# Optimization experiments

Measured on AMD Instinct MI355X. Metric: run time of the kernel, lower is better.

Reference implementation:

```python
import jax, jax.numpy as jnp
import numpy as np

N = 100000      # nodes
E = 1600000     # edges (before self-loops)
F_DIM = 256     # feat_dim
H = 64          # hidden_dim
EPS = 1e-5      # BatchNorm eps
NEG_SLOPE = 0.2 # PyG GATConv leaky_relu slope


def _glorot(key, shape):
    fan_in, fan_out = shape[0], shape[-1]
    s = jnp.sqrt(2.0 / (fan_in + fan_out)).astype(jnp.float32)
    return jax.random.normal(key, shape, dtype=jnp.float32) * s


def setup_inputs() -> dict:
    key = jax.random.key(0)
    ks = jax.random.split(key, 16)
    inp = {
        "feat": jax.random.normal(ks[0], (N, F_DIM), dtype=jnp.float32),
        "edge_index": jax.random.randint(ks[1], (2, E), 0, N, dtype=jnp.int64)
        if jax.config.jax_enable_x64 else jax.random.randint(ks[1], (2, E), 0, N).astype(jnp.int32),
    }
    dims = [(F_DIM, H), (H, H), (H, H), (H, F_DIM)]  # gc1-enc, gc2-enc, gc1-dec, gc2-dec
    for i, (din, dout) in enumerate(dims, start=1):
        k = jax.random.split(ks[1 + i], 4)
        inp[f"W{i}"] = _glorot(k[0], (din, dout))
        inp[f"as{i}"] = _glorot(k[1], (dout,))
        inp[f"ad{i}"] = _glorot(k[2], (dout,))
        inp[f"bi{i}"] = jnp.zeros((dout,), dtype=jnp.float32)
    # BatchNorm affine params (eval mode: running_mean=0, running_var=1)
    for i in range(1, 4):
        inp[f"g{i}"] = jnp.ones((H,), dtype=jnp.float32)
        inp[f"be{i}"] = jnp.zeros((H,), dtype=jnp.float32)
    return inp


def _gat(x, src, dst, W, a_src, a_dst, b, n):
    # PyG single-head GATConv: h = xW; e_ij = LeakyReLU(a_s.h_i + a_d.h_j);
    # alpha = softmax over edges sharing a destination; out_j = sum alpha_ij h_i + b
    h = x @ W                                   # [N, dout]
    e = jax.nn.leaky_relu((h @ a_src)[src] + (h @ a_dst)[dst], NEG_SLOPE)  # [Etot]
    m = jax.ops.segment_max(e, dst, num_segments=n)
    m = jnp.where(jnp.isfinite(m), m, 0.0)
    p = jnp.exp(e - m[dst])
    denom = jax.ops.segment_sum(p, dst, num_segments=n)
    alpha = p / (denom[dst] + 1e-16)
    out = jax.ops.segment_sum(alpha[:, None] * h[src], dst, num_segments=n)
    return out + b


def _bn_eval(x, gamma, beta):
    # eval-mode BatchNorm1d with running_mean=0, running_var=1
    return x * (gamma / jnp.sqrt(1.0 + EPS)) + beta


def reference(feat, edge_index,
              W1, as1, ad1, bi1, W2, as2, ad2, bi2,
              W3, as3, ad3, bi3, W4, as4, ad4, bi4,
              g1, be1, g2, be2, g3, be3):
    n = feat.shape[0]
    loops = jnp.arange(n, dtype=edge_index.dtype)
    src = jnp.concatenate([edge_index[0], loops])  # add_self_loops=True
    dst = jnp.concatenate([edge_index[1], loops])
    # GraphEncoder
    x = jax.nn.relu(_gat(feat, src, dst, W1, as1, ad1, bi1, n))
    x = _bn_eval(x, g1, be1)  # dropout inactive (eval)
    x = jax.nn.relu(_gat(x, src, dst, W2, as2, ad2, bi2, n))
    x = _bn_eval(x, g2, be2)
    # AttributeDecoder
    x = jax.nn.relu(_gat(x, src, dst, W3, as3, ad3, bi3, n))
    x = _bn_eval(x, g3, be3)
    x = jax.nn.relu(_gat(x, src, dst, W4, as4, ad4, bi4, n))
    return x
```

## Files before the change

kernel.cpp:

```cpp
#include <hip/hip_runtime.h>
#include <cmath>

#define SLOPE 0.2f
#define EPSV 1e-5f

__global__ __launch_bounds__(256) void deg_init_kernel(int* __restrict__ deg, int n) {
    int i = blockIdx.x * 256 + threadIdx.x;
    if (i <= n) deg[i] = (i < n) ? 1 : 0;
}

__global__ __launch_bounds__(256) void hist_kernel(const int* __restrict__ dst, int E,
                                                   int* __restrict__ deg) {
    int stride = gridDim.x * 256;
    for (int e = blockIdx.x * 256 + threadIdx.x; e < E; e += stride)
        atomicAdd(&deg[dst[e]], 1);
}

__global__ __launch_bounds__(256) void scan_block_kernel(const int* __restrict__ deg,
                                                         int* __restrict__ row,
                                                         int* __restrict__ partials, int n1) {
    __shared__ int s[256];
    int t = threadIdx.x;
    int i = blockIdx.x * 256 + t;
    int v = (i < n1) ? deg[i] : 0;
    s[t] = v;
    __syncthreads();
    for (int off = 1; off < 256; off <<= 1) {
        int x = (t >= off) ? s[t - off] : 0;
        __syncthreads();
        s[t] += x;
        __syncthreads();
    }
    if (i < n1) row[i] = s[t] - v;
    if (t == 255) partials[blockIdx.x] = s[255];
}

__global__ __launch_bounds__(1024) void scan_top_kernel(int* __restrict__ partials, int nb) {
    __shared__ int s[1024];
    int t = threadIdx.x;
    int v = (t < nb) ? partials[t] : 0;
    s[t] = v;
    __syncthreads();
    for (int off = 1; off < 1024; off <<= 1) {
        int x = (t >= off) ? s[t - off] : 0;
        __syncthreads();
        s[t] += x;
        __syncthreads();
    }
    if (t < nb) partials[t] = s[t] - v;
}

__global__ __launch_bounds__(256) void scan_add_kernel(int* __restrict__ row,
                                                       const int* __restrict__ partials, int n1) {
    int i = blockIdx.x * 256 + threadIdx.x;
    if (i < n1) row[i] += partials[blockIdx.x];
}

__global__ __launch_bounds__(256) void fill_self_kernel(const int* __restrict__ row,
                                                        int* __restrict__ cursor,
                                                        int* __restrict__ csr, int n) {
    int i = blockIdx.x * 256 + threadIdx.x;
    if (i < n) {
        int p = row[i];
        csr[p] = i;
        cursor[i] = p + 1;
    }
}

__global__ __launch_bounds__(256) void fill_edge_kernel(const int* __restrict__ src,
                                                        const int* __restrict__ dst, int E,
                                                        int* __restrict__ cursor,
                                                        int* __restrict__ csr) {
    int stride = gridDim.x * 256;
    for (int e = blockIdx.x * 256 + threadIdx.x; e < E; e += stride) {
        int p = atomicAdd(&cursor[dst[e]], 1);
        csr[p] = src[e];
    }
}

template <int DIN>
__device__ __forceinline__ float dot1(const float* __restrict__ Ws,
                                      const float* __restrict__ X, int node, int lane) {
    const float4* xr = reinterpret_cast<const float4*>(X + (size_t)node * DIN);
    float acc = 0.f;
#pragma unroll 8
    for (int k4 = 0; k4 < DIN / 4; ++k4) {
        float4 x4 = xr[k4];
        acc = fmaf(x4.x, Ws[(4 * k4 + 0) * 64 + lane], acc);
        acc = fmaf(x4.y, Ws[(4 * k4 + 1) * 64 + lane], acc);
        acc = fmaf(x4.z, Ws[(4 * k4 + 2) * 64 + lane], acc);
        acc = fmaf(x4.w, Ws[(4 * k4 + 3) * 64 + lane], acc);
    }
    return acc;
}

template <int DIN>
__global__ __launch_bounds__(256) void gemm_scores_kernel(
    const float* __restrict__ X, const float* __restrict__ W,
    const float* __restrict__ a_s, const float* __restrict__ a_d,
    float* __restrict__ H, float* __restrict__ s_src, float* __restrict__ s_dst, int n) {
    __shared__ float Ws[DIN * 64];
    const float4* W4 = reinterpret_cast<const float4*>(W);
    float4* Ws4 = reinterpret_cast<float4*>(Ws);
    for (int i = threadIdx.x; i < DIN * 16; i += 256) Ws4[i] = W4[i];
    __syncthreads();

    const int lane = threadIdx.x & 63;
    const int wv = threadIdx.x >> 6;
    const float as_l = a_s[lane];
    const float ad_l = a_d[lane];
    const int stride = gridDim.x * 16;

    for (int base = (blockIdx.x * 4 + wv) * 4; base < n; base += stride) {
        if (base + 4 <= n) {
            const float4* x0 = reinterpret_cast<const float4*>(X + (size_t)(base + 0) * DIN);
            const float4* x1 = reinterpret_cast<const float4*>(X + (size_t)(base + 1) * DIN);
            const float4* x2 = reinterpret_cast<const float4*>(X + (size_t)(base + 2) * DIN);
            const float4* x3 = reinterpret_cast<const float4*>(X + (size_t)(base + 3) * DIN);
            float acc0 = 0.f, acc1 = 0.f, acc2 = 0.f, acc3 = 0.f;
#pragma unroll 8
            for (int k4 = 0; k4 < DIN / 4; ++k4) {
                float4 a = x0[k4], b = x1[k4], c = x2[k4], d = x3[k4];
                float w0 = Ws[(4 * k4 + 0) * 64 + lane];
                float w1 = Ws[(4 * k4 + 1) * 64 + lane];
                float w2 = Ws[(4 * k4 + 2) * 64 + lane];
                float w3 = Ws[(4 * k4 + 3) * 64 + lane];
                acc0 = fmaf(a.x, w0, fmaf(a.y, w1, fmaf(a.z, w2, fmaf(a.w, w3, acc0))));
                acc1 = fmaf(b.x, w0, fmaf(b.y, w1, fmaf(b.z, w2, fmaf(b.w, w3, acc1))));
                acc2 = fmaf(c.x, w0, fmaf(c.y, w1, fmaf(c.z, w2, fmaf(c.w, w3, acc2))));
                acc3 = fmaf(d.x, w0, fmaf(d.y, w1, fmaf(d.z, w2, fmaf(d.w, w3, acc3))));
            }
            H[(size_t)(base + 0) * 64 + lane] = acc0;
            H[(size_t)(base + 1) * 64 + lane] = acc1;
            H[(size_t)(base + 2) * 64 + lane] = acc2;
            H[(size_t)(base + 3) * 64 + lane] = acc3;
            float p0s = acc0 * as_l, p0d = acc0 * ad_l;
            float p1s = acc1 * as_l, p1d = acc1 * ad_l;
            float p2s = acc2 * as_l, p2d = acc2 * ad_l;
            float p3s = acc3 * as_l, p3d = acc3 * ad_l;
#pragma unroll
            for (int off = 32; off; off >>= 1) {
                p0s += __shfl_xor(p0s, off); p0d += __shfl_xor(p0d, off);
                p1s += __shfl_xor(p1s, off); p1d += __shfl_xor(p1d, off);
                p2s += __shfl_xor(p2s, off); p2d += __shfl_xor(p2d, off);
                p3s += __shfl_xor(p3s, off); p3d += __shfl_xor(p3d, off);
            }
            if (lane == 0) {
                s_src[base + 0] = p0s; s_dst[base + 0] = p0d;
                s_src[base + 1] = p1s; s_dst[base + 1] = p1d;
                s_src[base + 2] = p2s; s_dst[base + 2] = p2d;
                s_src[base + 3] = p3s; s_dst[base + 3] = p3d;
            }
        } else {
            for (int node = base; node < n; ++node) {
                float acc = dot1<DIN>(Ws, X, node, lane);
                H[(size_t)node * 64 + lane] = acc;
                float ps = acc * as_l, pd = acc * ad_l;
#pragma unroll
                for (int off = 32; off; off >>= 1) {
                    ps += __shfl_xor(ps, off);
                    pd += __shfl_xor(pd, off);
                }
                if (lane == 0) { s_src[node] = ps; s_dst[node] = pd; }
            }
        }
    }
}

__global__ __launch_bounds__(256) void scores_x_kernel(
    const float* __restrict__ X, const float* __restrict__ Was,
    const float* __restrict__ Wad, float* __restrict__ s_src,
    float* __restrict__ s_dst, int n) {
    const int lane = threadIdx.x & 63;
    const int node = (blockIdx.x * 256 + threadIdx.x) >> 6;
    if (node >= n) return;
    float x = X[(size_t)node * 64 + lane];
    float ps = x * Was[lane];
    float pd = x * Wad[lane];
#pragma unroll
    for (int off = 32; off; off >>= 1) {
        ps += __shfl_xor(ps, off);
        pd += __shfl_xor(pd, off);
    }
    if (lane == 0) {
        s_src[node] = ps;
        s_dst[node] = pd;
    }
}

__global__ __launch_bounds__(128) void wa_kernel(const float* __restrict__ W ,
                                                 const float* __restrict__ a_s,
                                                 const float* __restrict__ a_d,
                                                 float* __restrict__ Was,
                                                 float* __restrict__ Wad) {
    int t = threadIdx.x;
    int k = t & 63;
    const float* a = (t < 64) ? a_s : a_d;
    float* o = (t < 64) ? Was : Wad;
    const float4* wr = reinterpret_cast<const float4*>(W + (size_t)k * 256);
    const float4* a4 = reinterpret_cast<const float4*>(a);
    float acc = 0.f;
#pragma unroll
    for (int j = 0; j < 64; ++j) {
        float4 w = wr[j];
        float4 av = a4[j];
        acc = fmaf(w.x, av.x, acc);
        acc = fmaf(w.y, av.y, acc);
        acc = fmaf(w.z, av.z, acc);
        acc = fmaf(w.w, av.w, acc);
    }
    o[k] = acc;
}

template <int MODE>
__global__ __launch_bounds__(256) void gather_kernel(
    const int* __restrict__ row, const int* __restrict__ csr,
    const float* __restrict__ s_src, const float* __restrict__ s_dst,
    const float* __restrict__ H, const float* __restrict__ bi,
    const float* __restrict__ g, const float* __restrict__ be,
    float* __restrict__ Out, int n) {
    const int lane = threadIdx.x & 63;
    const int node = (blockIdx.x * 256 + threadIdx.x) >> 6;
    if (node >= n) return;
    const int beg = row[node];
    const int end = row[node + 1];
    const int deg = end - beg;
    const float sdd = s_dst[node];

    const int e0 = beg + lane;
    int c0 = 0;
    float v0 = -1e30f;
    bool has0 = (e0 < end);
    if (has0) {
        c0 = csr[e0];
        float t = s_src[c0] + sdd;
        v0 = t >= 0.f ? t : SLOPE * t;
    }
    float m = v0;
    float dl = has0 ? 1.f : 0.f;
    for (int e = e0 + 64; e < end; e += 64) {
        int s = csr[e];
        float t = s_src[s] + sdd;
        t = t >= 0.f ? t : SLOPE * t;
        float nm = fmaxf(m, t);
        dl = dl * __expf(m - nm) + __expf(t - nm);
        m = nm;
    }
    float M = m;
#pragma unroll
    for (int off = 32; off; off >>= 1) M = fmaxf(M, __shfl_xor(M, off));
    dl *= __expf(m - M);
#pragma unroll
    for (int off = 32; off; off >>= 1) dl += __shfl_xor(dl, off);
    const float invden = 1.f / (dl + 1e-16f);
    const float p0 = has0 ? __expf(v0 - M) : 0.f;

    float acc = 0.f;
    const int nf = deg < 64 ? deg : 64;
    int k = 0;
    for (; k + 8 <= nf; k += 8) {
        int s0 = __shfl(c0, k + 0), s1 = __shfl(c0, k + 1);
        int s2 = __shfl(c0, k + 2), s3 = __shfl(c0, k + 3);
        int s4 = __shfl(c0, k + 4), s5 = __shfl(c0, k + 5);
        int s6 = __shfl(c0, k + 6), s7 = __shfl(c0, k + 7);
        float a0 = __shfl(p0, k + 0), a1 = __shfl(p0, k + 1);
        float a2 = __shfl(p0, k + 2), a3 = __shfl(p0, k + 3);
        float a4 = __shfl(p0, k + 4), a5 = __shfl(p0, k + 5);
        float a6 = __shfl(p0, k + 6), a7 = __shfl(p0, k + 7);
        float h0 = H[(size_t)s0 * 64 + lane], h1 = H[(size_t)s1 * 64 + lane];
        float h2 = H[(size_t)s2 * 64 + lane], h3 = H[(size_t)s3 * 64 + lane];
        float h4 = H[(size_t)s4 * 64 + lane], h5 = H[(size_t)s5 * 64 + lane];
        float h6 = H[(size_t)s6 * 64 + lane], h7 = H[(size_t)s7 * 64 + lane];
        acc = fmaf(a0, h0, acc); acc = fmaf(a1, h1, acc);
        acc = fmaf(a2, h2, acc); acc = fmaf(a3, h3, acc);
        acc = fmaf(a4, h4, acc); acc = fmaf(a5, h5, acc);
        acc = fmaf(a6, h6, acc); acc = fmaf(a7, h7, acc);
    }
    for (; k < nf; ++k) {
        int s = __shfl(c0, k);
        float a = __shfl(p0, k);
        acc = fmaf(a, H[(size_t)s * 64 + lane], acc);
    }
    for (int e = beg + 64; e < end; ++e) {
        int s = csr[e];
        float t = s_src[s] + sdd;
        t = t >= 0.f ? t : SLOPE * t;
        acc = fmaf(__expf(t - M), H[(size_t)s * 64 + lane], acc);
    }
    acc *= invden;

    float o;
    if (MODE == 0) {
        o = fmaxf(acc + bi[lane], 0.f) * (g[lane] * rsqrtf(1.f + EPSV)) + be[lane];
    } else {
        o = acc;
    }
    Out[(size_t)node * 64 + lane] = o;
}

__global__ __launch_bounds__(256) void gemm_out_kernel(const float* __restrict__ X,
                                                       const float* __restrict__ W,
                                                       const float* __restrict__ bi,
                                                       float* __restrict__ Out, int n) {
    const int j = threadIdx.x;
    float wcol[64];
#pragma unroll
    for (int k = 0; k < 64; ++k) wcol[k] = W[k * 256 + j];
    const float bj = bi[j];
    for (int node = blockIdx.x; node < n; node += gridDim.x) {
        const float4* xr = reinterpret_cast<const float4*>(X + (size_t)node * 64);
        float acc = 0.f;
#pragma unroll
        for (int k4 = 0; k4 < 16; ++k4) {
            float4 x4 = xr[k4];
            acc = fmaf(x4.x, wcol[4 * k4 + 0],
                  fmaf(x4.y, wcol[4 * k4 + 1],
                  fmaf(x4.z, wcol[4 * k4 + 2],
                  fmaf(x4.w, wcol[4 * k4 + 3], acc))));
        }
        Out[(size_t)node * 256 + j] = fmaxf(acc + bj, 0.f);
    }
}

extern "C" void kernel_launch(void* const* d_in, const int* in_sizes, int n_in,
                              void* d_out, int out_size, void* d_ws,
                              size_t ws_size, hipStream_t stream) {
    const float* feat = (const float*)d_in[0];
    const int* eidx = (const int*)d_in[1];
    const float* W[4] = {(const float*)d_in[2], (const float*)d_in[6],
                         (const float*)d_in[10], (const float*)d_in[14]};
    const float* As[4] = {(const float*)d_in[3], (const float*)d_in[7],
                          (const float*)d_in[11], (const float*)d_in[15]};
    const float* Ad[4] = {(const float*)d_in[4], (const float*)d_in[8],
                          (const float*)d_in[12], (const float*)d_in[16]};
    const float* Bi[4] = {(const float*)d_in[5], (const float*)d_in[9],
                          (const float*)d_in[13], (const float*)d_in[17]};
    const float* G[3] = {(const float*)d_in[18], (const float*)d_in[20],
                         (const float*)d_in[22]};
    const float* Be[3] = {(const float*)d_in[19], (const float*)d_in[21],
                          (const float*)d_in[23]};

    const int N = in_sizes[0] / 256;
    const int E = in_sizes[1] / 2;
    const int* srcA = eidx;
    const int* dstA = eidx + E;

    float* h = (float*)d_ws;
    float* xA = h + (size_t)N * 64;
    float* xB = xA + (size_t)N * 64;
    float* s_src = xB + (size_t)N * 64;
    float* s_dst = s_src + N;
    float* Was = s_dst + N;
    float* Wad = Was + 64;
    int* deg = (int*)(Wad + 64);
    int* row = deg + (N + 1);
    int* cursor = row + (N + 1);
    int* partials = cursor + N;
    int* csr = partials + 1024;

    const int n1 = N + 1;
    const int NB1 = (n1 + 255) / 256;
    const int node_grid = (N + 3) / 4;
    (void)ws_size; (void)n_in; (void)out_size;

    deg_init_kernel<<<NB1, 256, 0, stream>>>(deg, N);
    hist_kernel<<<2048, 256, 0, stream>>>(dstA, E, deg);
    scan_block_kernel<<<NB1, 256, 0, stream>>>(deg, row, partials, n1);
    scan_top_kernel<<<1, 1024, 0, stream>>>(partials, NB1);
    scan_add_kernel<<<NB1, 256, 0, stream>>>(row, partials, n1);
    fill_self_kernel<<<NB1, 256, 0, stream>>>(row, cursor, csr, N);
    fill_edge_kernel<<<2048, 256, 0, stream>>>(srcA, dstA, E, cursor, csr);

    gemm_scores_kernel<256><<<512, 256, 0, stream>>>(
        feat, W[0], As[0], Ad[0], h, s_src, s_dst, N);
    gather_kernel<0><<<node_grid, 256, 0, stream>>>(
        row, csr, s_src, s_dst, h, Bi[0], G[0], Be[0], xA, N);

    gemm_scores_kernel<64><<<1024, 256, 0, stream>>>(
        xA, W[1], As[1], Ad[1], h, s_src, s_dst, N);
    gather_kernel<0><<<node_grid, 256, 0, stream>>>(
        row, csr, s_src, s_dst, h, Bi[1], G[1], Be[1], xB, N);

    gemm_scores_kernel<64><<<1024, 256, 0, stream>>>(
        xB, W[2], As[2], Ad[2], h, s_src, s_dst, N);
    gather_kernel<0><<<node_grid, 256, 0, stream>>>(
        row, csr, s_src, s_dst, h, Bi[2], G[2], Be[2], xA, N);

    wa_kernel<<<1, 128, 0, stream>>>(W[3], As[3], Ad[3], Was, Wad);
    scores_x_kernel<<<node_grid, 256, 0, stream>>>(xA, Was, Wad, s_src, s_dst, N);
    gather_kernel<1><<<node_grid, 256, 0, stream>>>(
        row, csr, s_src, s_dst, xA, nullptr, nullptr, nullptr, h, N);
    gemm_out_kernel<<<2048, 256, 0, stream>>>(h, W[3], Bi[3], (float*)d_out, N);
}
```

Baseline: 1.108 ms.

## Hold weight columns in registers and split K across waves in layer-1 GEMM

The GEMM+score kernels now keep each lane's 64-entry weight column in registers instead of reading it from LDS. For the 256-wide first layer, each of the four waves handles a 64-wide K slice, and the partial sums are reduced through shared memory, with two barriers per group of 4 nodes. The aim is to remove LDS read traffic and let the weights fit in registers. The cost is higher register pressure, which may lower occupancy, plus extra syncs in the layer-1 kernel, whose grid is raised to 1024 blocks.

After: 1.126 ms. Within noise of the previous version (+1.6%).

```diff
diff --git a/kernel.cpp b/kernel.cpp
--- a/kernel.cpp
+++ b/kernel.cpp
@@ -78,66 +78,98 @@
     }
 }
 
-template <int DIN>
-__device__ __forceinline__ float dot1(const float* __restrict__ Ws,
-                                      const float* __restrict__ X, int node, int lane) {
-    const float4* xr = reinterpret_cast<const float4*>(X + (size_t)node * DIN);
-    float acc = 0.f;
-#pragma unroll 8
-    for (int k4 = 0; k4 < DIN / 4; ++k4) {
-        float4 x4 = xr[k4];
-        acc = fmaf(x4.x, Ws[(4 * k4 + 0) * 64 + lane], acc);
-        acc = fmaf(x4.y, Ws[(4 * k4 + 1) * 64 + lane], acc);
-        acc = fmaf(x4.z, Ws[(4 * k4 + 2) * 64 + lane], acc);
-        acc = fmaf(x4.w, Ws[(4 * k4 + 3) * 64 + lane], acc);
-    }
-    return acc;
-}
-
-template <int DIN>
-__global__ __launch_bounds__(256) void gemm_scores_kernel(
+__global__ __launch_bounds__(256) void gemm_scores256_kernel(
     const float* __restrict__ X, const float* __restrict__ W,
     const float* __restrict__ a_s, const float* __restrict__ a_d,
     float* __restrict__ H, float* __restrict__ s_src, float* __restrict__ s_dst, int n) {
-    __shared__ float Ws[DIN * 64];
-    const float4* W4 = reinterpret_cast<const float4*>(W);
-    float4* Ws4 = reinterpret_cast<float4*>(Ws);
-    for (int i = threadIdx.x; i < DIN * 16; i += 256) Ws4[i] = W4[i];
-    __syncthreads();
-
+    __shared__ float part[4 * 4 * 64];
     const int lane = threadIdx.x & 63;
     const int wv = threadIdx.x >> 6;
+    float wcol[64];
+#pragma unroll
+    for (int k = 0; k < 64; ++k) wcol[k] = W[(wv * 64 + k) * 64 + lane];
     const float as_l = a_s[lane];
     const float ad_l = a_d[lane];
-    const int stride = gridDim.x * 16;
-
-    for (int base = (blockIdx.x * 4 + wv) * 4; base < n; base += stride) {
+
+    for (int base = blockIdx.x * 4; base < n; base += gridDim.x * 4) {
+#pragma unroll
+        for (int g = 0; g < 4; ++g) {
+            const int node = base + g;
+            float acc = 0.f;
+            if (node < n) {
+                const float4* xr =
+                    reinterpret_cast<const float4*>(X + (size_t)node * 256 + wv * 64);
+#pragma unroll
+                for (int k4 = 0; k4 < 16; ++k4) {
+                    float4 x4 = xr[k4];
+                    acc = fmaf(x4.x, wcol[4 * k4 + 0],
+                          fmaf(x4.y, wcol[4 * k4 + 1],
+                          fmaf(x4.z, wcol[4 * k4 + 2],
+                          fmaf(x4.w, wcol[4 * k4 + 3], acc))));
+                }
+            }
+            part[(g * 4 + wv) * 64 + lane] = acc;
+        }
+        __syncthreads();
+        const int node = base + wv;
+        if (node < n) {
+            float h = part[(wv * 4 + 0) * 64 + lane] + part[(wv * 4 + 1) * 64 + lane] +
+                      part[(wv * 4 + 2) * 64 + lane] + part[(wv * 4 + 3) * 64 + lane];
+            H[(size_t)node * 64 + lane] = h;
+            float ps = h * as_l, pd = h * ad_l;
+#pragma unroll
+            for (int off = 32; off; off >>= 1) {
+                ps += __shfl_xor(ps, off);
+                pd += __shfl_xor(pd, off);
+            }
+            if (lane == 0) {
+                s_src[node] = ps;
+                s_dst[node] = pd;
+            }
+        }
+        __syncthreads();
+    }
+}
+
+__global__ __launch_bounds__(256) void gemm_scores64_kernel(
+    const float* __restrict__ X, const float* __restrict__ W,
+    const float* __restrict__ a_s, const float* __restrict__ a_d,
+    float* __restrict__ H, float* __restrict__ s_src, float* __restrict__ s_dst, int n) {
+    const int lane = threadIdx.x & 63;
+    const int wv = threadIdx.x >> 6;
+    float wcol[64];
+#pragma unroll
+    for (int k = 0; k < 64; ++k) wcol[k] = W[k * 64 + lane];
+    const float as_l = a_s[lane];
+    const float ad_l = a_d[lane];
+    const int wid = blockIdx.x * 4 + wv;
+    const int nw = gridDim.x * 4;
+
+    for (int base = wid * 4; base < n; base += nw * 4) {
         if (base + 4 <= n) {
-            const float4* x0 = reinterpret_cast<const float4*>(X + (size_t)(base + 0) * DIN);
-            const float4* x1 = reinterpret_cast<const float4*>(X + (size_t)(base + 1) * DIN);
-            const float4* x2 = reinterpret_cast<const float4*>(X + (size_t)(base + 2) * DIN);
-            const float4* x3 = reinterpret_cast<const float4*>(X + (size_t)(base + 3) * DIN);
-            float acc0 = 0.f, acc1 = 0.f, acc2 = 0.f, acc3 = 0.f;
-#pragma unroll 8
-            for (int k4 = 0; k4 < DIN / 4; ++k4) {
-                float4 a = x0[k4], b = x1[k4], c = x2[k4], d = x3[k4];
-                float w0 = Ws[(4 * k4 + 0) * 64 + lane];
-                float w1 = Ws[(4 * k4 + 1) * 64 + lane];
-                float w2 = Ws[(4 * k4 + 2) * 64 + lane];
-                float w3 = Ws[(4 * k4 + 3) * 64 + lane];
-                acc0 = fmaf(a.x, w0, fmaf(a.y, w1, fmaf(a.z, w2, fmaf(a.w, w3, acc0))));
-                acc1 = fmaf(b.x, w0, fmaf(b.y, w1, fmaf(b.z, w2, fmaf(b.w, w3, acc1))));
-                acc2 = fmaf(c.x, w0, fmaf(c.y, w1, fmaf(c.z, w2, fmaf(c.w, w3, acc2))));
-                acc3 = fmaf(d.x, w0, fmaf(d.y, w1, fmaf(d.z, w2, fmaf(d.w, w3, acc3))));
-            }
-            H[(size_t)(base + 0) * 64 + lane] = acc0;
-            H[(size_t)(base + 1) * 64 + lane] = acc1;
-            H[(size_t)(base + 2) * 64 + lane] = acc2;
-            H[(size_t)(base + 3) * 64 + lane] = acc3;
-            float p0s = acc0 * as_l, p0d = acc0 * ad_l;
-            float p1s = acc1 * as_l, p1d = acc1 * ad_l;
-            float p2s = acc2 * as_l, p2d = acc2 * ad_l;
-            float p3s = acc3 * as_l, p3d = acc3 * ad_l;
+            const float4* x0 = reinterpret_cast<const float4*>(X + (size_t)(base + 0) * 64);
+            const float4* x1 = reinterpret_cast<const float4*>(X + (size_t)(base + 1) * 64);
+            const float4* x2 = reinterpret_cast<const float4*>(X + (size_t)(base + 2) * 64);
+            const float4* x3 = reinterpret_cast<const float4*>(X + (size_t)(base + 3) * 64);
+            float a0 = 0.f, a1 = 0.f, a2 = 0.f, a3 = 0.f;
+#pragma unroll
+            for (int k4 = 0; k4 < 16; ++k4) {
+                float4 xa = x0[k4], xb = x1[k4], xc = x2[k4], xd = x3[k4];
+                float w0 = wcol[4 * k4 + 0], w1 = wcol[4 * k4 + 1];
+                float w2 = wcol[4 * k4 + 2], w3 = wcol[4 * k4 + 3];
+                a0 = fmaf(xa.x, w0, fmaf(xa.y, w1, fmaf(xa.z, w2, fmaf(xa.w, w3, a0))));
+                a1 = fmaf(xb.x, w0, fmaf(xb.y, w1, fmaf(xb.z, w2, fmaf(xb.w, w3, a1))));
+                a2 = fmaf(xc.x, w0, fmaf(xc.y, w1, fmaf(xc.z, w2, fmaf(xc.w, w3, a2))));
+                a3 = fmaf(xd.x, w0, fmaf(xd.y, w1, fmaf(xd.z, w2, fmaf(xd.w, w3, a3))));
+            }
+            H[(size_t)(base + 0) * 64 + lane] = a0;
+            H[(size_t)(base + 1) * 64 + lane] = a1;
+            H[(size_t)(base + 2) * 64 + lane] = a2;
+            H[(size_t)(base + 3) * 64 + lane] = a3;
+            float p0s = a0 * as_l, p0d = a0 * ad_l;
+            float p1s = a1 * as_l, p1d = a1 * ad_l;
+            float p2s = a2 * as_l, p2d = a2 * ad_l;
+            float p3s = a3 * as_l, p3d = a3 * ad_l;
 #pragma unroll
             for (int off = 32; off; off >>= 1) {
                 p0s += __shfl_xor(p0s, off); p0d += __shfl_xor(p0d, off);
@@ -153,7 +185,16 @@
             }
         } else {
             for (int node = base; node < n; ++node) {
-                float acc = dot1<DIN>(Ws, X, node, lane);
+                const float4* xr = reinterpret_cast<const float4*>(X + (size_t)node * 64);
+                float acc = 0.f;
+#pragma unroll
+                for (int k4 = 0; k4 < 16; ++k4) {
+                    float4 x4 = xr[k4];
+                    acc = fmaf(x4.x, wcol[4 * k4 + 0],
+                          fmaf(x4.y, wcol[4 * k4 + 1],
+                          fmaf(x4.z, wcol[4 * k4 + 2],
+                          fmaf(x4.w, wcol[4 * k4 + 3], acc))));
+                }
                 H[(size_t)node * 64 + lane] = acc;
                 float ps = acc * as_l, pd = acc * ad_l;
 #pragma unroll
@@ -371,17 +412,17 @@
     fill_self_kernel<<<NB1, 256, 0, stream>>>(row, cursor, csr, N);
     fill_edge_kernel<<<2048, 256, 0, stream>>>(srcA, dstA, E, cursor, csr);
 
-    gemm_scores_kernel<256><<<512, 256, 0, stream>>>(
+    gemm_scores256_kernel<<<1024, 256, 0, stream>>>(
         feat, W[0], As[0], Ad[0], h, s_src, s_dst, N);
     gather_kernel<0><<<node_grid, 256, 0, stream>>>(
         row, csr, s_src, s_dst, h, Bi[0], G[0], Be[0], xA, N);
 
-    gemm_scores_kernel<64><<<1024, 256, 0, stream>>>(
+    gemm_scores64_kernel<<<1024, 256, 0, stream>>>(
         xA, W[1], As[1], Ad[1], h, s_src, s_dst, N);
     gather_kernel<0><<<node_grid, 256, 0, stream>>>(
         row, csr, s_src, s_dst, h, Bi[1], G[1], Be[1], xB, N);
 
-    gemm_scores_kernel<64><<<1024, 256, 0, stream>>>(
+    gemm_scores64_kernel<<<1024, 256, 0, stream>>>(
         xB, W[2], As[2], Ad[2], h, s_src, s_dst, N);
     gather_kernel<0><<<node_grid, 256, 0, stream>>>(
         row, csr, s_src, s_dst, h, Bi[2], G[2], Be[2], xA, N);
```

## Hold weight columns in registers and tile 16 nodes per wave in GEMMs

Applied to the files above, without the earlier changes.

The dense projection kernels change from staging W in LDS across 256-thread blocks to single-wave blocks. Each block keeps a 64-row slice of a weight column in registers and computes 16 nodes at once, with K tiled for the 256-wide input. The output GEMM is restructured the same way, looping over four 64-column quarters per 16-node group. The aim is to drop LDS reads and block syncs and reuse register weights across nodes, at the cost of heavy register pressure, reloading weights per block, and many tiny blocks.

Result: slower. 1.205 ms (+8.8%).

```diff
diff --git a/kernel.cpp b/kernel.cpp
--- a/kernel.cpp
+++ b/kernel.cpp
@@ -78,91 +78,59 @@
     }
 }
 
-template <int DIN>
-__device__ __forceinline__ float dot1(const float* __restrict__ Ws,
-                                      const float* __restrict__ X, int node, int lane) {
-    const float4* xr = reinterpret_cast<const float4*>(X + (size_t)node * DIN);
-    float acc = 0.f;
-#pragma unroll 8
-    for (int k4 = 0; k4 < DIN / 4; ++k4) {
-        float4 x4 = xr[k4];
-        acc = fmaf(x4.x, Ws[(4 * k4 + 0) * 64 + lane], acc);
-        acc = fmaf(x4.y, Ws[(4 * k4 + 1) * 64 + lane], acc);
-        acc = fmaf(x4.z, Ws[(4 * k4 + 2) * 64 + lane], acc);
-        acc = fmaf(x4.w, Ws[(4 * k4 + 3) * 64 + lane], acc);
-    }
-    return acc;
-}
-
-template <int DIN>
-__global__ __launch_bounds__(256) void gemm_scores_kernel(
+template <int KTILES>
+__global__ __launch_bounds__(64, 4) void gemm_scores_kernel(
     const float* __restrict__ X, const float* __restrict__ W,
     const float* __restrict__ a_s, const float* __restrict__ a_d,
-    float* __restrict__ H, float* __restrict__ s_src, float* __restrict__ s_dst, int n) {
-    __shared__ float Ws[DIN * 64];
-    const float4* W4 = reinterpret_cast<const float4*>(W);
-    float4* Ws4 = reinterpret_cast<float4*>(Ws);
-    for (int i = threadIdx.x; i < DIN * 16; i += 256) Ws4[i] = W4[i];
-    __syncthreads();
-
-    const int lane = threadIdx.x & 63;
-    const int wv = threadIdx.x >> 6;
-    const float as_l = a_s[lane];
-    const float ad_l = a_d[lane];
-    const int stride = gridDim.x * 16;
-
-    for (int base = (blockIdx.x * 4 + wv) * 4; base < n; base += stride) {
-        if (base + 4 <= n) {
-            const float4* x0 = reinterpret_cast<const float4*>(X + (size_t)(base + 0) * DIN);
-            const float4* x1 = reinterpret_cast<const float4*>(X + (size_t)(base + 1) * DIN);
-            const float4* x2 = reinterpret_cast<const float4*>(X + (size_t)(base + 2) * DIN);
-            const float4* x3 = reinterpret_cast<const float4*>(X + (size_t)(base + 3) * DIN);
-            float acc0 = 0.f, acc1 = 0.f, acc2 = 0.f, acc3 = 0.f;
-#pragma unroll 8
-            for (int k4 = 0; k4 < DIN / 4; ++k4) {
-                float4 a = x0[k4], b = x1[k4], c = x2[k4], d = x3[k4];
-                float w0 = Ws[(4 * k4 + 0) * 64 + lane];
-                float w1 = Ws[(4 * k4 + 1) * 64 + lane];
-                float w2 = Ws[(4 * k4 + 2) * 64 + lane];
-                float w3 = Ws[(4 * k4 + 3) * 64 + lane];
-                acc0 = fmaf(a.x, w0, fmaf(a.y, w1, fmaf(a.z, w2, fmaf(a.w, w3, acc0))));
-                acc1 = fmaf(b.x, w0, fmaf(b.y, w1, fmaf(b.z, w2, fmaf(b.w, w3, acc1))));
-                acc2 = fmaf(c.x, w0, fmaf(c.y, w1, fmaf(c.z, w2, fmaf(c.w, w3, acc2))));
-                acc3 = fmaf(d.x, w0, fmaf(d.y, w1, fmaf(d.z, w2, fmaf(d.w, w3, acc3))));
+    float* __restrict__ H, float* __restrict__ s_src, float* __restrict__ s_dst,
+    int n) {
+    const int lane = threadIdx.x;
+    const int base = blockIdx.x * 16;
+    if (base >= n) return;
+
+    float acc[16];
+#pragma unroll
+    for (int g = 0; g < 16; ++g) acc[g] = 0.f;
+
+#pragma unroll 1
+    for (int t = 0; t < KTILES; ++t) {
+        float wcol[64];
+#pragma unroll
+        for (int k = 0; k < 64; ++k) wcol[k] = W[(t * 64 + k) * 64 + lane];
+#pragma unroll
+        for (int g = 0; g < 16; ++g) {
+            const int node = base + g;
+            if (node < n) {
+                const float4* xr = reinterpret_cast<const float4*>(
+                    X + (size_t)node * (KTILES * 64) + t * 64);
+#pragma unroll
+                for (int k4 = 0; k4 < 16; ++k4) {
+                    float4 x4 = xr[k4];
+                    acc[g] = fmaf(x4.x, wcol[4 * k4 + 0],
+                             fmaf(x4.y, wcol[4 * k4 + 1],
+                             fmaf(x4.z, wcol[4 * k4 + 2],
+                             fmaf(x4.w, wcol[4 * k4 + 3], acc[g]))));
+                }
             }
-            H[(size_t)(base + 0) * 64 + lane] = acc0;
-            H[(size_t)(base + 1) * 64 + lane] = acc1;
-            H[(size_t)(base + 2) * 64 + lane] = acc2;
-            H[(size_t)(base + 3) * 64 + lane] = acc3;
-            float p0s = acc0 * as_l, p0d = acc0 * ad_l;
-            float p1s = acc1 * as_l, p1d = acc1 * ad_l;
-            float p2s = acc2 * as_l, p2d = acc2 * ad_l;
-            float p3s = acc3 * as_l, p3d = acc3 * ad_l;
-#pragma unroll
-            for (int off = 32; off; off >>= 1) {
-                p0s += __shfl_xor(p0s, off); p0d += __shfl_xor(p0d, off);
-                p1s += __shfl_xor(p1s, off); p1d += __shfl_xor(p1d, off);
-                p2s += __shfl_xor(p2s, off); p2d += __shfl_xor(p2d, off);
-                p3s += __shfl_xor(p3s, off); p3d += __shfl_xor(p3d, off);
-            }
-            if (lane == 0) {
-                s_src[base + 0] = p0s; s_dst[base + 0] = p0d;
-                s_src[base + 1] = p1s; s_dst[base + 1] = p1d;
-                s_src[base + 2] = p2s; s_dst[base + 2] = p2d;
-                s_src[base + 3] = p3s; s_dst[base + 3] = p3d;
-            }
-        } else {
-            for (int node = base; node < n; ++node) {
-                float acc = dot1<DIN>(Ws, X, node, lane);
-                H[(size_t)node * 64 + lane] = acc;
-                float ps = acc * as_l, pd = acc * ad_l;
-#pragma unroll
-                for (int off = 32; off; off >>= 1) {
-                    ps += __shfl_xor(ps, off);
-                    pd += __shfl_xor(pd, off);
-                }
-                if (lane == 0) { s_src[node] = ps; s_dst[node] = pd; }
-            }
+        }
+    }
+
+    const float as_l = a_s[lane], ad_l = a_d[lane];
+#pragma unroll
+    for (int g = 0; g < 16; ++g) {
+        const int node = base + g;
+        if (node >= n) break;
+        float h = acc[g];
+        H[(size_t)node * 64 + lane] = h;
+        float ps = h * as_l, pd = h * ad_l;
+#pragma unroll
+        for (int off = 32; off; off >>= 1) {
+            ps += __shfl_xor(ps, off);
+            pd += __shfl_xor(pd, off);
+        }
+        if (lane == 0) {
+            s_src[node] = ps;
+            s_dst[node] = pd;
         }
     }
 }
@@ -298,27 +266,35 @@
     Out[(size_t)node * 64 + lane] = o;
 }
 
-__global__ __launch_bounds__(256) void gemm_out_kernel(const float* __restrict__ X,
-                                                       const float* __restrict__ W,
-                                                       const float* __restrict__ bi,
-                                                       float* __restrict__ Out, int n) {
-    const int j = threadIdx.x;
-    float wcol[64];
-#pragma unroll
-    for (int k = 0; k < 64; ++k) wcol[k] = W[k * 256 + j];
-    const float bj = bi[j];
-    for (int node = blockIdx.x; node < n; node += gridDim.x) {
-        const float4* xr = reinterpret_cast<const float4*>(X + (size_t)node * 64);
-        float acc = 0.f;
-#pragma unroll
-        for (int k4 = 0; k4 < 16; ++k4) {
-            float4 x4 = xr[k4];
-            acc = fmaf(x4.x, wcol[4 * k4 + 0],
-                  fmaf(x4.y, wcol[4 * k4 + 1],
-                  fmaf(x4.z, wcol[4 * k4 + 2],
-                  fmaf(x4.w, wcol[4 * k4 + 3], acc))));
+__global__ __launch_bounds__(64, 4) void gemm_out_kernel(const float* __restrict__ X,
+                                                         const float* __restrict__ W,
+                                                         const float* __restrict__ bi,
+                                                         float* __restrict__ Out, int n) {
+    const int lane = threadIdx.x;
+    const int base = blockIdx.x * 16;
+    if (base >= n) return;
+#pragma unroll 1
+    for (int q = 0; q < 4; ++q) {
+        float wcol[64];
+#pragma unroll
+        for (int k = 0; k < 64; ++k) wcol[k] = W[k * 256 + q * 64 + lane];
+        const float bj = bi[q * 64 + lane];
+#pragma unroll
+        for (int g = 0; g < 16; ++g) {
+            const int node = base + g;
+            if (node >= n) break;
+            const float4* xr = reinterpret_cast<const float4*>(X + (size_t)node * 64);
+            float acc = 0.f;
+#pragma unroll
+            for (int k4 = 0; k4 < 16; ++k4) {
+                float4 x4 = xr[k4];
+                acc = fmaf(x4.x, wcol[4 * k4 + 0],
+                      fmaf(x4.y, wcol[4 * k4 + 1],
+                      fmaf(x4.z, wcol[4 * k4 + 2],
+                      fmaf(x4.w, wcol[4 * k4 + 3], acc))));
+            }
+            Out[(size_t)node * 256 + q * 64 + lane] = fmaxf(acc + bj, 0.f);
         }
-        Out[(size_t)node * 256 + j] = fmaxf(acc + bj, 0.f);
     }
 }
 
@@ -361,6 +337,7 @@
     const int n1 = N + 1;
     const int NB1 = (n1 + 255) / 256;
     const int node_grid = (N + 3) / 4;
+    const int gemm_grid = (N + 15) / 16;
     (void)ws_size; (void)n_in; (void)out_size;
 
     deg_init_kernel<<<NB1, 256, 0, stream>>>(deg, N);
@@ -371,17 +348,17 @@
     fill_self_kernel<<<NB1, 256, 0, stream>>>(row, cursor, csr, N);
     fill_edge_kernel<<<2048, 256, 0, stream>>>(srcA, dstA, E, cursor, csr);
 
-    gemm_scores_kernel<256><<<512, 256, 0, stream>>>(
+    gemm_scores_kernel<4><<<gemm_grid, 64, 0, stream>>>(
         feat, W[0], As[0], Ad[0], h, s_src, s_dst, N);
     gather_kernel<0><<<node_grid, 256, 0, stream>>>(
         row, csr, s_src, s_dst, h, Bi[0], G[0], Be[0], xA, N);
 
-    gemm_scores_kernel<64><<<1024, 256, 0, stream>>>(
+    gemm_scores_kernel<1><<<gemm_grid, 64, 0, stream>>>(
         xA, W[1], As[1], Ad[1], h, s_src, s_dst, N);
     gather_kernel<0><<<node_grid, 256, 0, stream>>>(
         row, csr, s_src, s_dst, h, Bi[1], G[1], Be[1], xB, N);
 
-    gemm_scores_kernel<64><<<1024, 256, 0, stream>>>(
+    gemm_scores_kernel<1><<<gemm_grid, 64, 0, stream>>>(
         xB, W[2], As[2], Ad[2], h, s_src, s_dst, N);
     gather_kernel<0><<<node_grid, 256, 0, stream>>>(
         row, csr, s_src, s_dst, h, Bi[2], G[2], Be[2], xA, N);
@@ -390,5 +367,5 @@
     scores_x_kernel<<<node_grid, 256, 0, stream>>>(xA, Was, Wad, s_src, s_dst, N);
     gather_kernel<1><<<node_grid, 256, 0, stream>>>(
         row, csr, s_src, s_dst, xA, nullptr, nullptr, nullptr, h, N);
-    gemm_out_kernel<<<2048, 256, 0, stream>>>(h, W[3], Bi[3], (float*)d_out, N);
-}
+    gemm_out_kernel<<<gemm_grid, 64, 0, stream>>>(h, W[3], Bi[3], (float*)d_out, N);
+}
```
